# Kernel tuning notes

Hardware: AMD Instinct MI355X
Metric: run time of the kernel (lower is better)

## Reference

```python
import jax, jax.numpy as jnp
import numpy as np

BASE = 512  # per-axis encoding base; coords and queries are all < 512
NEG_FILL = -1000.0


def _encode(c):
    # c: [..., 4] int32 coords laid out as (x, y, z, batch)
    c = c.astype(jnp.int32)
    # max key = 3*512^3 + 511*(512^2+512+1) < 2^31, fits int32
    return ((c[..., 3] * BASE + c[..., 0]) * BASE + c[..., 1]) * BASE + c[..., 2]


def setup_inputs() -> dict:
    G, B, N, C, M_cap = 128, 4, 400000, 64, 360000
    rng = np.random.default_rng(0)
    # unique active voxels in a B x G^3 grid (torchsparse assumes unique coords)
    flat = rng.choice(B * G * G * G, size=N, replace=False)
    b = flat // (G * G * G)
    rem = flat % (G * G * G)
    x = rem // (G * G)
    y = (rem // G) % G
    z = rem % G
    coords = np.stack([x, y, z, b], axis=1).astype(np.int32)
    # spdownsample(stride=2, minkowski): unique floor-divided coords
    coarse = coords.copy()
    coarse[:, :3] //= 2
    out = np.unique(coarse, axis=0)
    if out.shape[0] >= M_cap:
        out = out[:M_cap]
    else:
        # pad with sentinel coords that can never match any input voxel
        pad = np.full((M_cap - out.shape[0], 4), 255, dtype=np.int32)
        pad[:, 3] = 0
        out = np.concatenate([out, pad], axis=0)
    feats = jax.random.normal(jax.random.key(0), (N, C), dtype=jnp.float32)
    return {
        "coords": jnp.asarray(coords),
        "feats": feats,
        "out_coords": jnp.asarray(out.astype(np.int32)),
    }


def reference(coords, feats, out_coords):
    N = coords.shape[0]
    M = out_coords.shape[0]
    # --- sphash(input.coords): sorted key table for exact-match lookup ---
    keys_in = _encode(coords)                      # [N]
    order = jnp.argsort(keys_in)                   # [N]
    skeys = keys_in[order]                         # [N] sorted
    # --- get_kernel_offsets(2,1,1): the 8 corners of the 2x2x2 kernel ---
    offs = jnp.stack(
        jnp.meshgrid(jnp.arange(2), jnp.arange(2), jnp.arange(2), indexing="ij"),
        axis=-1,
    ).reshape(8, 3)                                 # [8,3] in {0,1}^3
    # --- sphash(out_coords*2 + offsets) ---
    q_xyz = out_coords[None, :, :3] * 2 + offs[:, None, :]          # [8,M,3]
    q_b = jnp.broadcast_to(out_coords[None, :, 3:4], (8, M, 1))     # [8,M,1]
    kq = _encode(jnp.concatenate([q_xyz, q_b], axis=-1))            # [8,M]
    # --- sphashquery: index of matching input coord, -1 if missing ---
    pos = jnp.searchsorted(skeys, kq)              # [8,M]
    posc = jnp.clip(pos, 0, N - 1)
    valid = (pos < N) & (skeys[posc] == kq)
    results = jnp.where(valid, order[posc], -1)    # [8,M]
    # --- gather with -1000 sentinel row, max over the 8 kernel taps ---
    feat_pad = jnp.concatenate(
        [jnp.full((1, feats.shape[1]), NEG_FILL, feats.dtype), feats], axis=0
    )
    out_feature = jnp.max(feat_pad[results + 1], axis=0)  # [M,C]
    return out_feature
```

## Files before the change

kernel.cpp:

```cpp
#include <hip/hip_runtime.h>

#define NEG_FILL -1000.0f


__global__ void scatter_direct(const int* __restrict__ coords,
                               int* __restrict__ table, int N) {
    int i = blockIdx.x * blockDim.x + threadIdx.x;
    if (i >= N) return;
    const int4 c = reinterpret_cast<const int4*>(coords)[i];
    int key = ((c.w * 128 + c.x) * 128 + c.y) * 128 + c.z;
    table[key] = i;
}

__global__ __launch_bounds__(256) void pool_direct(
        const int* __restrict__ out_coords,
        const float* __restrict__ feats,
        const int* __restrict__ table,
        float* __restrict__ out, int M) {
    int tid = blockIdx.x * blockDim.x + threadIdx.x;
    int row = tid >> 4;
    if (row >= M) return;
    int lane = threadIdx.x & 63;
    int grp  = lane & 48;
    int cg   = (tid & 15) << 2;

    const int4 oc = reinterpret_cast<const int4*>(out_coords)[row];
    int bx = oc.x * 2, by = oc.y * 2, bz = oc.z * 2, b = oc.w;

    bool rowok = ((unsigned)(bx | by | bz) < 128u);
    int base = ((b * 128 + bx) * 128 + by) * 128 + bz;
    base = rowok ? base : 0;

    int o   = lane & 7;
    int off = ((o >> 2) << 14) + (((o >> 1) & 1) << 7) + (o & 1);
    int e   = table[base + off];

    bool myvalid = rowok && (e >= 0);
    unsigned long long bal = __ballot(myvalid);
    unsigned m = (unsigned)(bal >> grp) & 0xFFu;

    float4 acc = make_float4(NEG_FILL, NEG_FILL, NEG_FILL, NEG_FILL);
    while (m) {
        int oo = __ffs(m) - 1;
        m &= m - 1;
        int idx = __shfl(e, grp + oo);
        const float4 v = *reinterpret_cast<const float4*>(
            feats + ((long)idx << 6) + cg);
        acc.x = fmaxf(acc.x, v.x);
        acc.y = fmaxf(acc.y, v.y);
        acc.z = fmaxf(acc.z, v.z);
        acc.w = fmaxf(acc.w, v.w);
    }
    *reinterpret_cast<float4*>(out + ((long)row << 6) + cg) = acc;
}


#define HCAP (1 << 20)
#define HMASK (HCAP - 1)

__global__ void scatter_hash(const int* __restrict__ coords,
                             int* __restrict__ hkeys, int* __restrict__ hvals,
                             int N) {
    int i = blockIdx.x * blockDim.x + threadIdx.x;
    if (i >= N) return;
    const int4 c = reinterpret_cast<const int4*>(coords)[i];
    int key = ((c.w * 128 + c.x) * 128 + c.y) * 128 + c.z;
    unsigned slot = ((unsigned)key * 2654435761u) & HMASK;
    while (true) {
        int prev = atomicCAS(&hkeys[slot], -1, key);
        if (prev == -1 || prev == key) { hvals[slot] = i; break; }
        slot = (slot + 1) & HMASK;
    }
}

__device__ __forceinline__ int hash_lookup(const int* __restrict__ hkeys,
                                           const int* __restrict__ hvals,
                                           int key) {
    unsigned slot = ((unsigned)key * 2654435761u) & HMASK;
    while (true) {
        int k = hkeys[slot];
        if (k == key) return hvals[slot];
        if (k == -1) return -1;
        slot = (slot + 1) & HMASK;
    }
}

__global__ void pool_hash(const int* __restrict__ out_coords,
                          const float* __restrict__ feats,
                          const int* __restrict__ hkeys,
                          const int* __restrict__ hvals,
                          float* __restrict__ out, int M) {
    int tid = blockIdx.x * blockDim.x + threadIdx.x;
    int row = tid >> 4;
    if (row >= M) return;
    int cg = (tid & 15) << 2;

    const int4 oc = reinterpret_cast<const int4*>(out_coords)[row];
    int bx = oc.x * 2, by = oc.y * 2, bz = oc.z * 2, b = oc.w;

    float4 acc = make_float4(NEG_FILL, NEG_FILL, NEG_FILL, NEG_FILL);

    if ((unsigned)(bx | by | bz) < 128u) {
        int base = ((b * 128 + bx) * 128 + by) * 128 + bz;
        #pragma unroll
        for (int o = 0; o < 8; ++o) {
            int key = base + (o >> 2) * (128 * 128) + ((o >> 1) & 1) * 128 + (o & 1);
            int idx = hash_lookup(hkeys, hvals, key);
            if (idx >= 0) {
                const float4 v = *reinterpret_cast<const float4*>(
                    feats + ((long)idx << 6) + cg);
                acc.x = fmaxf(acc.x, v.x);
                acc.y = fmaxf(acc.y, v.y);
                acc.z = fmaxf(acc.z, v.z);
                acc.w = fmaxf(acc.w, v.w);
            }
        }
    }
    *reinterpret_cast<float4*>(out + ((long)row << 6) + cg) = acc;
}

extern "C" void kernel_launch(void* const* d_in, const int* in_sizes, int n_in,
                              void* d_out, int out_size, void* d_ws, size_t ws_size,
                              hipStream_t stream) {
    const int*   coords     = (const int*)d_in[0];
    const float* feats      = (const float*)d_in[1];
    const int*   out_coords = (const int*)d_in[2];
    float*       out        = (float*)d_out;

    int N = in_sizes[0] / 4;
    int M = in_sizes[2] / 4;

    const size_t TABLE_BYTES = (size_t)4 * 128 * 128 * 128 * sizeof(int);

    if (ws_size >= TABLE_BYTES) {
        int* table = (int*)d_ws;
        hipMemsetAsync(table, 0xFF, TABLE_BYTES, stream);
        scatter_direct<<<(N + 255) / 256, 256, 0, stream>>>(coords, table, N);
        pool_direct<<<((M * 16) + 255) / 256, 256, 0, stream>>>(
            out_coords, feats, table, out, M);
    } else {
        int* hkeys = (int*)d_ws;
        int* hvals = hkeys + HCAP;
        hipMemsetAsync(hkeys, 0xFF, (size_t)HCAP * sizeof(int), stream);
        scatter_hash<<<(N + 255) / 256, 256, 0, stream>>>(coords, hkeys, hvals, N);
        pool_hash<<<((M * 16) + 255) / 256, 256, 0, stream>>>(
            out_coords, feats, hkeys, hvals, out, M);
    }
}
```

Before: 58.56 us.

## Process four output rows per 8-lane group with batched table lookups

The pooling kernel now gives each output row 8 lanes instead of 16, and each lane loads two float4 channel chunks. Each 8-lane group handles ROWS=4 rows strided by Q, and all four coordinate loads and table lookups are issued before the gather loops. This raises memory-level parallelism and removes the duplicate table lookups that the 16-lane layout did for each row. In exchange it launches fewer threads, uses more registers per thread, and serializes the per-row gathers inside each thread.

```diff
diff --git a/kernel.cpp b/kernel.cpp
--- a/kernel.cpp
+++ b/kernel.cpp
@@ -1,6 +1,7 @@
 #include <hip/hip_runtime.h>
 
 #define NEG_FILL -1000.0f
+#define ROWS 4
 
 
 __global__ void scatter_direct(const int* __restrict__ coords,
@@ -16,42 +17,61 @@
         const int* __restrict__ out_coords,
         const float* __restrict__ feats,
         const int* __restrict__ table,
-        float* __restrict__ out, int M) {
-    int tid = blockIdx.x * blockDim.x + threadIdx.x;
-    int row = tid >> 4;
-    if (row >= M) return;
+        float* __restrict__ out, int M, int Q) {
+    int tid  = blockIdx.x * blockDim.x + threadIdx.x;
+    int slot = tid >> 3;
+    if (slot >= Q) return;
     int lane = threadIdx.x & 63;
-    int grp  = lane & 48;
-    int cg   = (tid & 15) << 2;
+    int o    = lane & 7;
+    int grp  = lane & 56;
+    int off  = ((o >> 2) << 14) + (((o >> 1) & 1) << 7) + (o & 1);
 
-    const int4 oc = reinterpret_cast<const int4*>(out_coords)[row];
-    int bx = oc.x * 2, by = oc.y * 2, bz = oc.z * 2, b = oc.w;
+    int  row[ROWS];
+    int4 oc[ROWS];
+    #pragma unroll
+    for (int r = 0; r < ROWS; ++r) {
+        row[r] = slot + r * Q;
+        int rr = row[r] < M ? row[r] : 0;
+        oc[r] = reinterpret_cast<const int4*>(out_coords)[rr];
+    }
 
-    bool rowok = ((unsigned)(bx | by | bz) < 128u);
-    int base = ((b * 128 + bx) * 128 + by) * 128 + bz;
-    base = rowok ? base : 0;
+    int  e[ROWS];
+    bool rowok[ROWS];
+    #pragma unroll
+    for (int r = 0; r < ROWS; ++r) {
+        int bx = oc[r].x * 2, by = oc[r].y * 2, bz = oc[r].z * 2, b = oc[r].w;
+        rowok[r] = ((unsigned)(bx | by | bz) < 128u) && (row[r] < M);
+        int base = ((b * 128 + bx) * 128 + by) * 128 + bz;
+        base = rowok[r] ? base : 0;
+        e[r] = table[base + off];
+    }
 
-    int o   = lane & 7;
-    int off = ((o >> 2) << 14) + (((o >> 1) & 1) << 7) + (o & 1);
-    int e   = table[base + off];
+    #pragma unroll
+    for (int r = 0; r < ROWS; ++r) {
+        unsigned long long bal = __ballot(rowok[r] && (e[r] >= 0));
+        unsigned m = (unsigned)(bal >> grp) & 0xFFu;
 
-    bool myvalid = rowok && (e >= 0);
-    unsigned long long bal = __ballot(myvalid);
-    unsigned m = (unsigned)(bal >> grp) & 0xFFu;
-
-    float4 acc = make_float4(NEG_FILL, NEG_FILL, NEG_FILL, NEG_FILL);
-    while (m) {
-        int oo = __ffs(m) - 1;
-        m &= m - 1;
-        int idx = __shfl(e, grp + oo);
-        const float4 v = *reinterpret_cast<const float4*>(
-            feats + ((long)idx << 6) + cg);
-        acc.x = fmaxf(acc.x, v.x);
-        acc.y = fmaxf(acc.y, v.y);
-        acc.z = fmaxf(acc.z, v.z);
-        acc.w = fmaxf(acc.w, v.w);
+        float4 a0 = make_float4(NEG_FILL, NEG_FILL, NEG_FILL, NEG_FILL);
+        float4 a1 = a0;
+        while (m) {
+            int oo = __ffs(m) - 1;
+            m &= m - 1;
+            int idx = __shfl(e[r], grp + oo);
+            const float4* fp = reinterpret_cast<const float4*>(
+                feats + ((long)idx << 6));
+            float4 v0 = fp[o];
+            float4 v1 = fp[8 + o];
+            a0.x = fmaxf(a0.x, v0.x); a0.y = fmaxf(a0.y, v0.y);
+            a0.z = fmaxf(a0.z, v0.z); a0.w = fmaxf(a0.w, v0.w);
+            a1.x = fmaxf(a1.x, v1.x); a1.y = fmaxf(a1.y, v1.y);
+            a1.z = fmaxf(a1.z, v1.z); a1.w = fmaxf(a1.w, v1.w);
+        }
+        if (row[r] < M) {
+            float4* op = reinterpret_cast<float4*>(out + ((long)row[r] << 6));
+            op[o]     = a0;
+            op[8 + o] = a1;
+        }
     }
-    *reinterpret_cast<float4*>(out + ((long)row << 6) + cg) = acc;
 }
 
 
@@ -136,8 +156,10 @@
         int* table = (int*)d_ws;
         hipMemsetAsync(table, 0xFF, TABLE_BYTES, stream);
         scatter_direct<<<(N + 255) / 256, 256, 0, stream>>>(coords, table, N);
-        pool_direct<<<((M * 16) + 255) / 256, 256, 0, stream>>>(
-            out_coords, feats, table, out, M);
+        int Q = (M + ROWS - 1) / ROWS;
+        int threads = Q * 8;
+        pool_direct<<<(threads + 255) / 256, 256, 0, stream>>>(
+            out_coords, feats, table, out, M, Q);
     } else {
         int* hkeys = (int*)d_ws;
         int* hvals = hkeys + HCAP;
```

After: 57.43 us. About the same (-1.9%).
